# Kernel tuning notes

Hardware: AMD Instinct MI355X
Metric: run time of the kernel (lower is better)

## Reference

```python
import jax, jax.numpy as jnp
import numpy as np

N = 50000      # nodes
E = 800000     # edges (avg degree 16)
IN = 128       # in_size
OUT = 64       # out_size
H = 32         # hidden_size
WIDTH = 3      # width
SCALE = 0.05


def _laplacian(x, src, tgt, n):
    # normalized Laplacian action: out[t] = sum_{edges into t} (x[t] - x[s]) / deg(t)
    deg = jax.ops.segment_sum(jnp.ones((tgt.shape[0],), x.dtype), tgt, num_segments=n)
    fac = 1.0 / deg[tgt]                       # [E], deg>=1 for any target that appears
    msg = (x[tgt] - x[src]) * fac[:, None]     # [E, F]
    return jax.ops.segment_sum(msg, tgt, num_segments=n)


def _grouped_linear(x, Wg, bg):
    # Conv1d(kernel=1, groups=width) == per-group linear
    n = x.shape[0]
    xg = x.reshape(n, WIDTH, -1)               # [N, width, h_in]
    out = jnp.einsum('nwh,who->nwo', xg, Wg) + bg
    return out.reshape(n, -1)                  # [N, width*h_out]


def setup_inputs() -> dict:
    key = jax.random.key(0)
    ks = jax.random.split(key, 14)
    data = jax.random.normal(ks[0], (N, IN), jnp.float32)
    src = jax.random.randint(ks[1], (E,), 0, N)
    tgt = jnp.sort(jax.random.randint(ks[2], (E,), 0, N))
    # preprocess ConvSkip: Linear(in, hidden*width) + Linear(in, hidden*width)
    W_pre = jax.random.normal(ks[3], (IN, H * WIDTH), jnp.float32) * SCALE
    b_pre = jnp.zeros((H * WIDTH,), jnp.float32)
    T_pre = jax.random.normal(ks[4], (IN, H * WIDTH), jnp.float32) * SCALE
    bT_pre = jnp.zeros((H * WIDTH,), jnp.float32)
    # middle WideConvSkip (depth-2 = 1 block): grouped conv [width, H, H]
    W_blk = jax.random.normal(ks[5], (WIDTH, H, H), jnp.float32) * SCALE
    b_blk = jnp.zeros((WIDTH, H), jnp.float32)
    T_blk = jax.random.normal(ks[6], (IN, H * WIDTH), jnp.float32) * SCALE
    bT_blk = jnp.zeros((H * WIDTH,), jnp.float32)
    # postprocess WideConvSkip: grouped conv [width, H, OUT]
    W_post = jax.random.normal(ks[7], (WIDTH, H, OUT), jnp.float32) * SCALE
    b_post = jnp.zeros((WIDTH, OUT), jnp.float32)
    T_post = jax.random.normal(ks[8], (IN, OUT * WIDTH), jnp.float32) * SCALE
    bT_post = jnp.zeros((OUT * WIDTH,), jnp.float32)
    return {"data": data, "src": src, "tgt": tgt,
            "W_pre": W_pre, "b_pre": b_pre, "T_pre": T_pre, "bT_pre": bT_pre,
            "W_blk": W_blk, "b_blk": b_blk, "T_blk": T_blk, "bT_blk": bT_blk,
            "W_post": W_post, "b_post": b_post, "T_post": T_post, "bT_post": bT_post}


def reference(data, src, tgt, W_pre, b_pre, T_pre, bT_pre,
              W_blk, b_blk, T_blk, bT_blk,
              W_post, b_post, T_post, bT_post):
    n = data.shape[0]
    # preprocess ConvSkip: sigma(L f(x) + g(x))
    out = data @ W_pre + b_pre
    out = _laplacian(out, src, tgt, n)
    out = jax.nn.relu(out + data @ T_pre + bT_pre)       # [N, H*width]
    # middle WideConvSkip (depth - 2 = 1)
    h = _grouped_linear(out, W_blk, b_blk)
    h = _laplacian(h, src, tgt, n)
    out = jax.nn.relu(h + data @ T_blk + bT_blk)          # [N, H*width]
    # postprocess WideConvSkip
    h = _grouped_linear(out, W_post, b_post)
    h = _laplacian(h, src, tgt, n)
    out = jax.nn.relu(h + data @ T_post + bT_post)        # [N, OUT*width]
    # reshape(N, -1, width) then adaptive_avg_pool1d(., 1) == mean over width
    out = out.reshape(n, -1, WIDTH)
    return out.mean(axis=-1, keepdims=True)               # [N, OUT, 1]
```

## Files before the change

### kernel.cpp

```cpp
#include <hip/hip_runtime.h>
#include <hip/hip_fp8.h>
#include <cstdint>
#include <cstddef>

#define N_NODES 50000
#define E_EDGES 800000
#define IN_F    128
#define PCOLS   512

typedef unsigned short ushortT;
typedef unsigned int   uintT;
typedef unsigned char  u8T;
typedef __attribute__((ext_vector_type(8))) short s8v;
typedef __attribute__((ext_vector_type(4))) float f4v;
typedef __attribute__((ext_vector_type(2))) float f2v;

__device__ __forceinline__ float bflo(uintT u){ union{uintT i;float f;}c; c.i=u<<16; return c.f; }
__device__ __forceinline__ float bfhi(uintT u){ union{uintT i;float f;}c; c.i=u&0xFFFF0000u; return c.f; }
__device__ __forceinline__ ushortT f2bfu(float f){
    union{float f;uintT u;}c; c.f=f;
    uintT r = c.u + 0x7FFF + ((c.u>>16)&1);
    return (ushortT)(r>>16);
}
__device__ __forceinline__ uintT pack2(float a, float b){
    return (uintT)f2bfu(a) | ((uintT)f2bfu(b) << 16);
}
__device__ __forceinline__ float f8f(uintT b){
    __hip_fp8_e4m3 h; h.__x = (__hip_fp8_storage_t)(b & 0xFF); return (float)h;
}
__device__ __forceinline__ uintT ff8(float f){
    __hip_fp8_e4m3 h(f); return (uintT)h.__x;
}
__device__ __forceinline__ f2v cvtpk_sw(uintT u, bool hi){
    uintT w = hi ? (u >> 16) : u;
    f2v r; r.x = f8f(w); r.y = f8f(w >> 8); return r;
}
#if defined(__has_builtin)
#if __has_builtin(__builtin_amdgcn_cvt_pk_f32_fp8)
#define CVTPK(u, hi) __builtin_amdgcn_cvt_pk_f32_fp8((u), (hi))
#else
#define CVTPK(u, hi) cvtpk_sw((u), (hi))
#endif
#else
#define CVTPK(u, hi) cvtpk_sw((u), (hi))
#endif

__global__ void prep1(const float* __restrict__ A,
                      const float* __restrict__ Wp,  const float* __restrict__ bp,
                      const float* __restrict__ Tp,  const float* __restrict__ bTp,
                      const float* __restrict__ Tb,  const float* __restrict__ bTb,
                      const float* __restrict__ Tpo, const float* __restrict__ bTpo,
                      const float* __restrict__ Wpost,
                      const int* __restrict__ tgt,
                      ushortT* __restrict__ Wb, float* __restrict__ bcat,
                      float2* __restrict__ Wp2,
                      ushortT* __restrict__ Ab, int* __restrict__ row_ptr,
                      u8T* __restrict__ rb1f8, u8T* __restrict__ rb2f8)
{
    int gid = blockIdx.x * 256 + threadIdx.x;
    {
        size_t off = (size_t)gid * 8;
        float4 v0 = *(const float4*)(A + off);
        float4 v1 = *(const float4*)(A + off + 4);
        uint4 u;
        u.x = pack2(v0.x, v0.y); u.y = pack2(v0.z, v0.w);
        u.z = pack2(v1.x, v1.y); u.w = pack2(v1.z, v1.w);
        *(uint4*)(Ab + off) = u;
    }
    if (gid < IN_F * PCOLS) {
        int k = gid >> 9;
        int c = gid & 511;
        float v;
        if      (c < 96)  v = Wp [k*96  + c];
        else if (c < 192) v = Tp [k*96  + (c-96)];
        else if (c < 288) v = Tb [k*96  + (c-192)];
        else if (c < 480) v = Tpo[k*192 + (c-288)];
        else              v = 0.f;
        Wb[(size_t)c*IN_F + k] = f2bfu(v);
        if (k == 0) {
            float b;
            if      (c < 96)  b = bp  [c];
            else if (c < 192) b = bTp [c-96];
            else if (c < 288) b = bTb [c-192];
            else if (c < 480) b = bTpo[c-288];
            else              b = 0.f;
            bcat[c] = b;
        }
        if (gid < 3*16*64) {
            int w = gid >> 10, r = gid & 1023;
            int i2 = r >> 6, j = r & 63;
            Wp2[gid] = make_float2(Wpost[(w*32 + 2*i2)*64 + j],
                                   Wpost[(w*32 + 2*i2 + 1)*64 + j]);
        }
    }
    if (gid < 24) {
        *(uintT*)(rb1f8 + (size_t)N_NODES*96 + 4*gid) = 0;
        *(uintT*)(rb2f8 + (size_t)N_NODES*96 + 4*gid) = 0;
    }
    if (gid <= N_NODES) {
        int lo = 0, hi = E_EDGES;
        while (lo < hi) {
            int mid = (lo + hi) >> 1;
            if (tgt[mid] < gid) lo = mid + 1; else hi = mid;
        }
        row_ptr[gid] = lo;
    }
}

__global__ __launch_bounds__(256, 4) void gemm_mfma(const ushortT* __restrict__ Ab,
                                                    const ushortT* __restrict__ Wb,
                                                    const float* __restrict__ bcat,
                                                    ushortT* __restrict__ Pb, int M)
{
    __shared__ ushortT Bsl[128][136];
    int tid = threadIdx.x;
    int i = blockIdx.x;
    int xcd = i & 7, j = i >> 3;
    int nb = (j & 3) * 128;
    int mb = (xcd * 49 + (j >> 2)) * 128;
    int wv = tid >> 6, lane = tid & 63;
    int wm = wv >> 1, wn = wv & 1;
    int cl = lane & 15, q = lane >> 4;

    #pragma unroll
    for (int r = 0; r < 8; ++r) {
        int idx = tid + 256*r;
        int row = idx >> 4, qq = idx & 15;
        uint4 v = *(const uint4*)(Wb + (size_t)(nb+row)*IN_F + qq*8);
        *(uint4*)(&Bsl[row][qq*8]) = v;
    }
    __syncthreads();

    f4v acc[4][4];
    #pragma unroll
    for (int a = 0; a < 4; ++a)
        #pragma unroll
        for (int b = 0; b < 4; ++b) acc[a][b] = (f4v)0.f;

    int gmBase = mb + wm*64;
    #pragma unroll
    for (int ks = 0; ks < 4; ++ks) {
        int ko = ks*32 + q*8;
        s8v af[4], bf[4];
        #pragma unroll
        for (int mt = 0; mt < 4; ++mt) {
            int gm = gmBase + mt*16 + cl;
            uint4 va = make_uint4(0,0,0,0);
            if (gm < M) va = *(const uint4*)(Ab + (size_t)gm*IN_F + ko);
            af[mt] = *(s8v*)&va;
        }
        #pragma unroll
        for (int nt = 0; nt < 4; ++nt)
            bf[nt] = *(const s8v*)(&Bsl[wn*64 + nt*16 + cl][ko]);
        #pragma unroll
        for (int mt = 0; mt < 4; ++mt)
            #pragma unroll
            for (int nt = 0; nt < 4; ++nt)
                acc[mt][nt] = __builtin_amdgcn_mfma_f32_16x16x32_bf16(af[mt], bf[nt], acc[mt][nt], 0, 0, 0);
    }

    __syncthreads();

    #pragma unroll
    for (int nt = 0; nt < 4; ++nt) {
        int cn = wn*64 + nt*16 + cl;
        float bv = bcat[nb + cn];
        #pragma unroll
        for (int mt = 0; mt < 4; ++mt) {
            int rm0 = wm*64 + mt*16 + q*4;
            #pragma unroll
            for (int r = 0; r < 4; ++r)
                Bsl[rm0 + r][cn] = f2bfu(acc[mt][nt][r] + bv);
        }
    }
    __syncthreads();

    #pragma unroll
    for (int p = 0; p < 8; ++p) {
        int idx = tid + 256*p;
        int row = idx >> 4, sg = idx & 15;
        int gm = mb + row;
        if (gm < M) {
            uint4 v = *(const uint4*)(&Bsl[row][sg*8]);
            *(uint4*)(Pb + (size_t)gm*PCOLS + nb + sg*8) = v;
        }
    }
}

__global__ void cvt_y0(const ushortT* __restrict__ Pb, u8T* __restrict__ Y8)
{
    int gid = blockIdx.x * 256 + threadIdx.x;
    if (gid < N_NODES*24) {
        int t = gid / 24, q = gid - t*24;
        uint2 rv = *(const uint2*)(Pb + (size_t)t*PCOLS + 4*q);
        uintT o = ff8(bflo(rv.x)) | (ff8(bfhi(rv.x)) << 8)
                | (ff8(bflo(rv.y)) << 16) | (ff8(bfhi(rv.y)) << 24);
        *(uintT*)(Y8 + (size_t)t*96 + 4*q) = o;
    } else if (gid < N_NODES*24 + 24) {
        *(uintT*)(Y8 + (size_t)N_NODES*96 + 4*(gid - N_NODES*24)) = 0;
    }
}

#define LANE_GEO8                                                                 \
    int lane = threadIdx.x & 63;                                                  \
    int pL = lane < 48 ? lane : 0;                                                \
    int lq = (lane < 24) ? lane : ((lane < 48) ? lane - 24 : lane - 48);          \
    int bpb = (lane >= 24 && lane < 48) ? 4 : 0;          \
    int in4 = 4*lq;

#define GPK_W(X8, sv, S0, CNT, u)                                                 \
    _Pragma("unroll")                                                             \
    for (int s_ = 0; s_ < (CNT); ++s_) {                                          \
        int vr_ = __builtin_amdgcn_ds_bpermute(bpb + 8*((S0)+s_), sv);            \
        u[s_] = *(const uintT*)((const u8T*)(X8) + (uintT)(vr_ + in4));           \
    }
#define GPK_D(u, CNT, a0, a1, b0, b1)                                             \
    _Pragma("unroll")                                                             \
    for (int s_ = 0; s_ < (CNT); ++s_) {                                          \
        f2v l_ = CVTPK(u[s_], 0);                                                 \
        f2v h_ = CVTPK(u[s_], 1);                                                 \
        if (s_ & 1) { b0 += l_; b1 += h_; } else { a0 += l_; a1 += h_; }          \
    }
#define GATHER_PK(X8, lo, deg, sv, sx, sy)                                        \
    float sx, sy;                                                                 \
    {                                                                             \
        f2v a0={0.f,0.f}, a1={0.f,0.f}, b0={0.f,0.f}, b1={0.f,0.f};               \
        uintT u[12];                                                              \
        GPK_W(X8, sv, 0, 12, u)                                                   \
        GPK_D(u, 12, a0, a1, b0, b1)                                              \
        if (deg > 24) {                                                           \
            GPK_W(X8, sv, 12, 12, u)                                              \
            GPK_D(u, 12, a0, a1, b0, b1)                                          \
        }                                                                         \
        if (deg > 48) {                                                           \
            GPK_W(X8, sv, 24, 8, u)                                               \
            GPK_D(u, 8, a0, a1, b0, b1)                                           \
        }                                                                         \
        if (deg > 64) {                                                           \
            _Pragma("unroll 1")                                                   \
            for (int j_ = lo + 64; j_ < lo + deg; ++j_) {                         \
                int off_ = src[j_] * 96;                                          \
                uintT t_ = *(const uintT*)((const u8T*)(X8) + (uintT)(off_ + in4));\
                if (lane < 24) { a0 += CVTPK(t_, 0); a1 += CVTPK(t_, 1); }        \
            }                                                                     \
        }                                                                         \
        f2v va = a0 + b0, vb = a1 + b1;        \
         \
        int pl_ = (lane < 24) ? lane + 24 : ((lane < 48) ? lane - 24 : lane);     \
        va.x += __shfl(va.x, pl_); va.y += __shfl(va.y, pl_);                     \
        vb.x += __shfl(vb.x, pl_); vb.y += __shfl(vb.y, pl_);                     \
        int fl_ = pL >> 1;                                                        \
        float e0_ = __shfl(va.x, fl_), e1_ = __shfl(va.y, fl_);                   \
        float e2_ = __shfl(vb.x, fl_), e3_ = __shfl(vb.y, fl_);                   \
        sx = (pL & 1) ? e2_ : e0_;                                                \
        sy = (pL & 1) ? e3_ : e1_;                                                \
    }

#define DESC4(t0)                                                                 \
    int lo0,dg0,sv0, lo1,dg1,sv1, lo2,dg2,sv2, lo3,dg3,sv3;                       \
    {                                                                             \
        int rA0 = row_ptr[(t0)];    int rB0 = row_ptr[(t0)+1];                    \
        int rA1 = row_ptr[(t0)+4];  int rB1 = row_ptr[(t0)+5];                    \
        int rA2 = row_ptr[(t0)+8];  int rB2 = row_ptr[(t0)+9];                    \
        int rA3 = row_ptr[(t0)+12]; int rB3 = row_ptr[(t0)+13];                   \
        lo0 = __builtin_amdgcn_readfirstlane(rA0);                                \
        dg0 = __builtin_amdgcn_readfirstlane(rB0) - lo0;                          \
        lo1 = __builtin_amdgcn_readfirstlane(rA1);                                \
        dg1 = __builtin_amdgcn_readfirstlane(rB1) - lo1;                          \
        lo2 = __builtin_amdgcn_readfirstlane(rA2);                                \
        dg2 = __builtin_amdgcn_readfirstlane(rB2) - lo2;                          \
        lo3 = __builtin_amdgcn_readfirstlane(rA3);                                \
        dg3 = __builtin_amdgcn_readfirstlane(rB3) - lo3;                          \
        int e0 = lo0 + lane; if (e0 > E_EDGES-1) e0 = E_EDGES-1;                  \
        int e1 = lo1 + lane; if (e1 > E_EDGES-1) e1 = E_EDGES-1;                  \
        int e2 = lo2 + lane; if (e2 > E_EDGES-1) e2 = E_EDGES-1;                  \
        int e3 = lo3 + lane; if (e3 > E_EDGES-1) e3 = E_EDGES-1;                  \
        int sn0 = src[e0]; int sn1 = src[e1];                                     \
        int sn2 = src[e2]; int sn3 = src[e3];                                     \
        sv0 = (lane < dg0 ? sn0 : N_NODES) * 96;                                  \
        sv1 = (lane < dg1 ? sn1 : N_NODES) * 96;                                  \
        sv2 = (lane < dg2 ? sn2 : N_NODES) * 96;                                  \
        sv3 = (lane < dg3 ? sn3 : N_NODES) * 96;                                  \
    }

__global__ __launch_bounds__(256) void lap1(
    const ushortT* __restrict__ Pb,
    const u8T*     __restrict__ Y8,
    const int* __restrict__ src, const int* __restrict__ row_ptr,
    ushortT* __restrict__ rb1, u8T* __restrict__ rb1f8)
{
    LANE_GEO8
    int wvw = threadIdx.x >> 6;
    int t0 = blockIdx.x*16 + wvw;
    DESC4(t0)

#define LAP1_IT(tt, lo, deg, sv)                                                  \
    {                                                                             \
        int t_ = __builtin_amdgcn_readfirstlane(tt);                              \
        uintT ux = *(const uintT*)(Pb + (size_t)t_*PCOLS + 2*pL);                 \
        uintT zu = *(const uintT*)(Pb + (size_t)t_*PCOLS + 96 + 2*pL);            \
        GATHER_PK(Y8, lo, deg, sv, sx, sy)                                        \
        float inv = (deg) > 0 ? 1.f/(float)(deg) : 0.f;                           \
        float mf  = (deg) > 0 ? 1.f : 0.f;                                        \
        if (lane < 48) {                                                          \
            float ox = fmaxf(mf*bflo(ux) - sx*inv + bflo(zu), 0.f);               \
            float oy = fmaxf(mf*bfhi(ux) - sy*inv + bfhi(zu), 0.f);               \
            *(uintT*)(rb1 + (size_t)t_*96 + 2*pL) = pack2(ox, oy);                \
            *(ushortT*)(rb1f8 + (size_t)t_*96 + 2*pL) =                           \
                (ushortT)(ff8(ox) | (ff8(oy) << 8));                              \
        }                                                                         \
    }
    LAP1_IT(t0,      lo0, dg0, sv0)
    LAP1_IT(t0 + 4,  lo1, dg1, sv1)
    LAP1_IT(t0 + 8,  lo2, dg2, sv2)
    LAP1_IT(t0 + 12, lo3, dg3, sv3)
#undef LAP1_IT
}

__global__ __launch_bounds__(256) void lap2(
    const ushortT* __restrict__ Xb,
    const u8T*     __restrict__ X8,
    const ushortT* __restrict__ Pb,
    const int* __restrict__ src, const int* __restrict__ row_ptr,
    const float* __restrict__ Wblk,
    ushortT* __restrict__ rb2, u8T* __restrict__ rb2f8)
{
    __shared__ float wS[3*32*32];
    for (int i = threadIdx.x; i < 3072; i += 256) wS[i] = Wblk[i];
    __syncthreads();

    LANE_GEO8
    int wvw = threadIdx.x >> 6;
    int w  = pL >> 4;
    int jj = pL & 15;
    const float2* wc = ((const float2*)wS) + (w*512 + jj);
    int t0 = blockIdx.x*16 + wvw;
    DESC4(t0)

#define LAP2_IT(tt, lo, deg, sv)                                                  \
    {                                                                             \
        int t_ = __builtin_amdgcn_readfirstlane(tt);                              \
        uintT ux = *(const uintT*)(Xb + (size_t)t_*96 + 2*pL);                    \
        uintT zu = *(const uintT*)(Pb + (size_t)t_*PCOLS + 192 + 2*pL);           \
        GATHER_PK(X8, lo, deg, sv, sx, sy)                                        \
        float inv = (deg) > 0 ? 1.f/(float)(deg) : 0.f;                           \
        float mf  = (deg) > 0 ? 1.f : 0.f;                                        \
        float Lx = mf*bflo(ux) - sx*inv;                                          \
        float Ly = mf*bfhi(ux) - sy*inv;                                          \
        float accx = 0.f, accy = 0.f;                                             \
        _Pragma("unroll")                                                         \
        for (int d = 0; d < 16; ++d) {                                            \
            int sl = w*16 + d;                                                    \
            float ax = __shfl(Lx, sl);                                            \
            float ay = __shfl(Ly, sl);                                            \
            float2 wa = wc[(2*d)*16];                                             \
            float2 wb = wc[(2*d+1)*16];                                           \
            accx = fmaf(ax, wa.x, accx); accx = fmaf(ay, wb.x, accx);             \
            accy = fmaf(ax, wa.y, accy); accy = fmaf(ay, wb.y, accy);             \
        }                                                                         \
        if (lane < 48) {                                                          \
            float ox = fmaxf(accx + bflo(zu), 0.f);                               \
            float oy = fmaxf(accy + bfhi(zu), 0.f);                               \
            *(uintT*)(rb2 + (size_t)t_*96 + 2*pL) = pack2(ox, oy);                \
            *(ushortT*)(rb2f8 + (size_t)t_*96 + 2*pL) =                           \
                (ushortT)(ff8(ox) | (ff8(oy) << 8));                              \
        }                                                                         \
    }
    LAP2_IT(t0,      lo0, dg0, sv0)
    LAP2_IT(t0 + 4,  lo1, dg1, sv1)
    LAP2_IT(t0 + 8,  lo2, dg2, sv2)
    LAP2_IT(t0 + 12, lo3, dg3, sv3)
#undef LAP2_IT
}

__global__ __launch_bounds__(256) void lap3(
    const ushortT* __restrict__ Xb,
    const u8T*     __restrict__ X8,
    const ushortT* __restrict__ Pb,
    const int* __restrict__ src, const int* __restrict__ row_ptr,
    const float2* __restrict__ Wp2,
    float* __restrict__ out)
{
    __shared__ float2 wS[3*16*64];
    __shared__ float  sm[4][96];
    for (int i = threadIdx.x; i < 3072; i += 256) wS[i] = Wp2[i];
    __syncthreads();

    LANE_GEO8
    int wvw = threadIdx.x >> 6;
    const float2* wl = wS + lane;
    int t0 = blockIdx.x*16 + wvw;
    DESC4(t0)

#define LAP3_IT(tt, lo, deg, sv)                                                  \
    {                                                                             \
        int t_ = __builtin_amdgcn_readfirstlane(tt);                              \
        uintT ux = *(const uintT*)(Xb + (size_t)t_*96 + 2*pL);                    \
        float z0 = bflo((uintT)Pb[(size_t)t_*PCOLS + 288 + lane]);                \
        float z1 = bflo((uintT)Pb[(size_t)t_*PCOLS + 352 + lane]);                \
        float z2 = bflo((uintT)Pb[(size_t)t_*PCOLS + 416 + lane]);                \
        GATHER_PK(X8, lo, deg, sv, sx, sy)                                        \
        float inv = (deg) > 0 ? 1.f/(float)(deg) : 0.f;                           \
        float mf  = (deg) > 0 ? 1.f : 0.f;                                        \
        float Lx = mf*bflo(ux) - sx*inv;                                          \
        float Ly = mf*bfhi(ux) - sy*inv;                                          \
        if (lane < 48) {                                                          \
            sm[wvw][2*pL]     = Lx;                                               \
            sm[wvw][2*pL + 1] = Ly;                                               \
        }                                                                         \
        __builtin_amdgcn_wave_barrier();                                          \
        float a0 = 0.f, a1 = 0.f, a2 = 0.f;                                       \
        _Pragma("unroll")                                                         \
        for (int w2 = 0; w2 < 3; ++w2) {                                          \
            float acc = 0.f;                                                      \
            _Pragma("unroll")                                                     \
            for (int i2 = 0; i2 < 16; ++i2) {                                     \
                float2 iv = *(const float2*)(&sm[wvw][w2*32 + 2*i2]);             \
                float2 p  = wl[(w2*16 + i2)*64];                                  \
                acc = fmaf(iv.x, p.x, acc);                                       \
                acc = fmaf(iv.y, p.y, acc);                                       \
            }                                                                     \
            if (w2 == 0) a0 = acc; else if (w2 == 1) a1 = acc; else a2 = acc;     \
        }                                                                         \
        __builtin_amdgcn_wave_barrier();                                          \
        float o0 = fmaxf(a0 + z0, 0.f);                                           \
        float o1 = fmaxf(a1 + z1, 0.f);                                           \
        float o2 = fmaxf(a2 + z2, 0.f);                                           \
        float r = 0.f;                                                            \
        _Pragma("unroll")                                                         \
        for (int q = 0; q < 3; ++q) {                                             \
            int c = 3*lane + q;                                                   \
            int sl = c & 63, wsel = c >> 6;                                       \
            float v0 = __shfl(o0, sl);                                            \
            float v1 = __shfl(o1, sl);                                            \
            float v2 = __shfl(o2, sl);                                            \
            r += (wsel == 0) ? v0 : ((wsel == 1) ? v1 : v2);                      \
        }                                                                         \
        out[(size_t)t_*64 + lane] = r * (1.0f/3.0f);                              \
    }
    LAP3_IT(t0,      lo0, dg0, sv0)
    LAP3_IT(t0 + 4,  lo1, dg1, sv1)
    LAP3_IT(t0 + 8,  lo2, dg2, sv2)
    LAP3_IT(t0 + 12, lo3, dg3, sv3)
#undef LAP3_IT
}

extern "C" void kernel_launch(void* const* d_in, const int* in_sizes, int n_in,
                              void* d_out, int out_size, void* d_ws, size_t ws_size,
                              hipStream_t stream)
{
    const float* data    = (const float*)d_in[0];
    const int*   src     = (const int*)  d_in[1];
    const int*   tgt     = (const int*)  d_in[2];
    const float* W_pre   = (const float*)d_in[3];
    const float* b_pre   = (const float*)d_in[4];
    const float* T_pre   = (const float*)d_in[5];
    const float* bT_pre  = (const float*)d_in[6];
    const float* W_blk   = (const float*)d_in[7];
    const float* b_blk   = (const float*)d_in[8];
    const float* T_blk   = (const float*)d_in[9];
    const float* bT_blk  = (const float*)d_in[10];
    const float* W_post  = (const float*)d_in[11];
    const float* b_post  = (const float*)d_in[12];
    const float* T_post  = (const float*)d_in[13];
    const float* bT_post = (const float*)d_in[14];
    float* out = (float*)d_out;

    float*   ws      = (float*)d_ws;
    float*   bcat    = ws;
    float2*  Wp2     = (float2*)(bcat + 512);
    int*     row_ptr = (int*)(Wp2 + 3*16*64);
    ushortT* Pb      = (ushortT*)(row_ptr + 50008);
    ushortT* rb1     = Pb  + (size_t)(N_NODES+1) * PCOLS;
    ushortT* rb2     = rb1 + (size_t)(N_NODES+1) * 96;
    ushortT* Ab      = rb2 + (size_t)(N_NODES+1) * 96;
    ushortT* Wb      = Ab  + (size_t)N_NODES * IN_F;
    u8T*     Y8      = (u8T*)(Wb + 512*IN_F);
    u8T*     rb1f8   = Y8  + (size_t)(N_NODES+1) * 96;
    u8T*     rb2f8   = rb1f8 + (size_t)(N_NODES+1) * 96;

    prep1<<<(N_NODES*IN_F/8)/256, 256, 0, stream>>>(
        data, W_pre, b_pre, T_pre, bT_pre, T_blk, bT_blk, T_post, bT_post,
        W_post, tgt, Wb, bcat, Wp2, Ab, row_ptr, rb1f8, rb2f8);

    gemm_mfma<<<1568, 256, 0, stream>>>(Ab, Wb, bcat, Pb, N_NODES);

    cvt_y0<<<(N_NODES*24 + 24 + 255)/256, 256, 0, stream>>>(Pb, Y8);

    lap1<<<N_NODES/16, 256, 0, stream>>>(Pb, Y8, src, row_ptr, rb1, rb1f8);
    lap2<<<N_NODES/16, 256, 0, stream>>>(rb1, rb1f8, Pb, src, row_ptr, W_blk, rb2, rb2f8);
    lap3<<<N_NODES/16, 256, 0, stream>>>(rb2, rb2f8, Pb, src, row_ptr, Wp2, out);
}
```

Measured before the change: 269.2 us.

## Precompute padded per-node neighbor offset table and simplify fp8 gather to readlane

Adds a build_svp kernel that builds a padded [N,64] table of source-row byte offsets once, so the three Laplacian kernels load it with a coalesced read instead of recomputing src lookups each time. The gather is also rewritten: the old version split each edge across lane halves using ds_bpermute plus shuffles, and the new one has each lane load 2 bytes per edge, taking the offset via readlane and looping in chunks of 16 up to the degree. This removes the cross-lane reduction shuffles, at the cost of more, narrower loads per lane, an extra kernel launch and a 12.8 MB table that must be written and read back.

```diff
diff --git a/kernel.cpp b/kernel.cpp
--- a/kernel.cpp
+++ b/kernel.cpp
@@ -107,6 +107,18 @@
     }
 }
 
+__global__ void build_svp(const int* __restrict__ src, const int* __restrict__ row_ptr,
+                          int* __restrict__ svp)
+{
+    int gid = blockIdx.x * 256 + threadIdx.x;
+    int t = gid >> 6, slot = gid & 63;
+    int lo = row_ptr[t];
+    int deg = row_ptr[t+1] - lo;
+    int e = lo + slot; if (e > E_EDGES - 1) e = E_EDGES - 1;
+    int v = slot < deg ? src[e] : N_NODES;
+    svp[gid] = v * 96;
+}
+
 __global__ __launch_bounds__(256, 4) void gemm_mfma(const ushortT* __restrict__ Ab,
                                                     const ushortT* __restrict__ Wb,
                                                     const float* __restrict__ bcat,
@@ -201,105 +213,79 @@
     }
 }
 
-#define LANE_GEO8                                                                 \
-    int lane = threadIdx.x & 63;                                                  \
-    int pL = lane < 48 ? lane : 0;                                                \
-    int lq = (lane < 24) ? lane : ((lane < 48) ? lane - 24 : lane - 48);          \
-    int bpb = (lane >= 24 && lane < 48) ? 4 : 0;          \
-    int in4 = 4*lq;
-
-#define GPK_W(X8, sv, S0, CNT, u)                                                 \
-    _Pragma("unroll")                                                             \
-    for (int s_ = 0; s_ < (CNT); ++s_) {                                          \
-        int vr_ = __builtin_amdgcn_ds_bpermute(bpb + 8*((S0)+s_), sv);            \
-        u[s_] = *(const uintT*)((const u8T*)(X8) + (uintT)(vr_ + in4));           \
-    }
-#define GPK_D(u, CNT, a0, a1, b0, b1)                                             \
-    _Pragma("unroll")                                                             \
-    for (int s_ = 0; s_ < (CNT); ++s_) {                                          \
-        f2v l_ = CVTPK(u[s_], 0);                                                 \
-        f2v h_ = CVTPK(u[s_], 1);                                                 \
-        if (s_ & 1) { b0 += l_; b1 += h_; } else { a0 += l_; a1 += h_; }          \
-    }
-#define GATHER_PK(X8, lo, deg, sv, sx, sy)                                        \
+#define GATHER96F8(X8, lo, deg, sv, pL, sx, sy)                                   \
     float sx, sy;                                                                 \
     {                                                                             \
-        f2v a0={0.f,0.f}, a1={0.f,0.f}, b0={0.f,0.f}, b1={0.f,0.f};               \
-        uintT u[12];                                                              \
-        GPK_W(X8, sv, 0, 12, u)                                                   \
-        GPK_D(u, 12, a0, a1, b0, b1)                                              \
-        if (deg > 24) {                                                           \
-            GPK_W(X8, sv, 12, 12, u)                                              \
-            GPK_D(u, 12, a0, a1, b0, b1)                                          \
-        }                                                                         \
-        if (deg > 48) {                                                           \
-            GPK_W(X8, sv, 24, 8, u)                                               \
-            GPK_D(u, 8, a0, a1, b0, b1)                                           \
+        f2v c0={0.f,0.f}, c1={0.f,0.f}, c2={0.f,0.f}, c3={0.f,0.f};               \
+        int dmax = deg < 64 ? deg : 64;                                           \
+        _Pragma("unroll 1")                                                       \
+        for (int w_ = 0; w_ < dmax; w_ += 16) {                                   \
+            uintT u[16];                                                          \
+            _Pragma("unroll")                                                     \
+            for (int kk = 0; kk < 16; ++kk) {                                     \
+                int off = __builtin_amdgcn_readlane(sv, w_ + kk);                 \
+                u[kk] = *(const ushortT*)((const u8T*)(X8) + off + 2*pL);         \
+            }                                                                     \
+            _Pragma("unroll")                                                     \
+            for (int kk = 0; kk < 16; ++kk) {                                     \
+                f2v v_ = CVTPK(u[kk], 0);                                         \
+                switch (kk & 3) {                                                 \
+                    case 0: c0 += v_; break;                                      \
+                    case 1: c1 += v_; break;                                      \
+                    case 2: c2 += v_; break;                                      \
+                    default:c3 += v_; break;                                      \
+                }                                                                 \
+            }                                                                     \
         }                                                                         \
         if (deg > 64) {                                                           \
             _Pragma("unroll 1")                                                   \
             for (int j_ = lo + 64; j_ < lo + deg; ++j_) {                         \
-                int off_ = src[j_] * 96;                                          \
-                uintT t_ = *(const uintT*)((const u8T*)(X8) + (uintT)(off_ + in4));\
-                if (lane < 24) { a0 += CVTPK(t_, 0); a1 += CVTPK(t_, 1); }        \
+                int off = src[j_] * 96;                                           \
+                uintT u0 = *(const ushortT*)((const u8T*)(X8) + off + 2*pL);      \
+                c0 += CVTPK(u0, 0);                                               \
             }                                                                     \
         }                                                                         \
-        f2v va = a0 + b0, vb = a1 + b1;        \
-         \
-        int pl_ = (lane < 24) ? lane + 24 : ((lane < 48) ? lane - 24 : lane);     \
-        va.x += __shfl(va.x, pl_); va.y += __shfl(va.y, pl_);                     \
-        vb.x += __shfl(vb.x, pl_); vb.y += __shfl(vb.y, pl_);                     \
-        int fl_ = pL >> 1;                                                        \
-        float e0_ = __shfl(va.x, fl_), e1_ = __shfl(va.y, fl_);                   \
-        float e2_ = __shfl(vb.x, fl_), e3_ = __shfl(vb.y, fl_);                   \
-        sx = (pL & 1) ? e2_ : e0_;                                                \
-        sy = (pL & 1) ? e3_ : e1_;                                                \
-    }
-
-#define DESC4(t0)                                                                 \
-    int lo0,dg0,sv0, lo1,dg1,sv1, lo2,dg2,sv2, lo3,dg3,sv3;                       \
-    {                                                                             \
-        int rA0 = row_ptr[(t0)];    int rB0 = row_ptr[(t0)+1];                    \
-        int rA1 = row_ptr[(t0)+4];  int rB1 = row_ptr[(t0)+5];                    \
-        int rA2 = row_ptr[(t0)+8];  int rB2 = row_ptr[(t0)+9];                    \
-        int rA3 = row_ptr[(t0)+12]; int rB3 = row_ptr[(t0)+13];                   \
-        lo0 = __builtin_amdgcn_readfirstlane(rA0);                                \
-        dg0 = __builtin_amdgcn_readfirstlane(rB0) - lo0;                          \
-        lo1 = __builtin_amdgcn_readfirstlane(rA1);                                \
-        dg1 = __builtin_amdgcn_readfirstlane(rB1) - lo1;                          \
-        lo2 = __builtin_amdgcn_readfirstlane(rA2);                                \
-        dg2 = __builtin_amdgcn_readfirstlane(rB2) - lo2;                          \
-        lo3 = __builtin_amdgcn_readfirstlane(rA3);                                \
-        dg3 = __builtin_amdgcn_readfirstlane(rB3) - lo3;                          \
-        int e0 = lo0 + lane; if (e0 > E_EDGES-1) e0 = E_EDGES-1;                  \
-        int e1 = lo1 + lane; if (e1 > E_EDGES-1) e1 = E_EDGES-1;                  \
-        int e2 = lo2 + lane; if (e2 > E_EDGES-1) e2 = E_EDGES-1;                  \
-        int e3 = lo3 + lane; if (e3 > E_EDGES-1) e3 = E_EDGES-1;                  \
-        int sn0 = src[e0]; int sn1 = src[e1];                                     \
-        int sn2 = src[e2]; int sn3 = src[e3];                                     \
-        sv0 = (lane < dg0 ? sn0 : N_NODES) * 96;                                  \
-        sv1 = (lane < dg1 ? sn1 : N_NODES) * 96;                                  \
-        sv2 = (lane < dg2 ? sn2 : N_NODES) * 96;                                  \
-        sv3 = (lane < dg3 ? sn3 : N_NODES) * 96;                                  \
-    }
+        f2v cs_ = (c0 + c1) + (c2 + c3);                                          \
+        sx = cs_.x; sy = cs_.y;                                                   \
+    }
+
+#define DESC_SVP(tB)                                                              \
+    int sv0 = svp[(size_t)((tB)     )*64 + lane];                                 \
+    int sv1 = svp[(size_t)((tB) +  4)*64 + lane];                                 \
+    int sv2 = svp[(size_t)((tB) +  8)*64 + lane];                                 \
+    int sv3 = svp[(size_t)((tB) + 12)*64 + lane];                                 \
+    int rA0 = row_ptr[(tB)];    int rB0 = row_ptr[(tB)+1];                        \
+    int rA1 = row_ptr[(tB)+4];  int rB1 = row_ptr[(tB)+5];                        \
+    int rA2 = row_ptr[(tB)+8];  int rB2 = row_ptr[(tB)+9];                        \
+    int rA3 = row_ptr[(tB)+12]; int rB3 = row_ptr[(tB)+13];                       \
+    int lo0 = __builtin_amdgcn_readfirstlane(rA0);                                \
+    int dg0 = __builtin_amdgcn_readfirstlane(rB0) - lo0;                          \
+    int lo1 = __builtin_amdgcn_readfirstlane(rA1);                                \
+    int dg1 = __builtin_amdgcn_readfirstlane(rB1) - lo1;                          \
+    int lo2 = __builtin_amdgcn_readfirstlane(rA2);                                \
+    int dg2 = __builtin_amdgcn_readfirstlane(rB2) - lo2;                          \
+    int lo3 = __builtin_amdgcn_readfirstlane(rA3);                                \
+    int dg3 = __builtin_amdgcn_readfirstlane(rB3) - lo3;
 
 __global__ __launch_bounds__(256) void lap1(
     const ushortT* __restrict__ Pb,
     const u8T*     __restrict__ Y8,
     const int* __restrict__ src, const int* __restrict__ row_ptr,
+    const int* __restrict__ svp,
     ushortT* __restrict__ rb1, u8T* __restrict__ rb1f8)
 {
-    LANE_GEO8
-    int wvw = threadIdx.x >> 6;
-    int t0 = blockIdx.x*16 + wvw;
-    DESC4(t0)
+    int lane = threadIdx.x & 63;
+    int wvw  = threadIdx.x >> 6;
+    int pL = lane < 48 ? lane : 0;
+    int tB = blockIdx.x*16 + wvw;
+    DESC_SVP(tB)
 
 #define LAP1_IT(tt, lo, deg, sv)                                                  \
     {                                                                             \
         int t_ = __builtin_amdgcn_readfirstlane(tt);                              \
         uintT ux = *(const uintT*)(Pb + (size_t)t_*PCOLS + 2*pL);                 \
         uintT zu = *(const uintT*)(Pb + (size_t)t_*PCOLS + 96 + 2*pL);            \
-        GATHER_PK(Y8, lo, deg, sv, sx, sy)                                        \
+        GATHER96F8(Y8, lo, deg, sv, pL, sx, sy)                                   \
         float inv = (deg) > 0 ? 1.f/(float)(deg) : 0.f;                           \
         float mf  = (deg) > 0 ? 1.f : 0.f;                                        \
         if (lane < 48) {                                                          \
@@ -310,10 +296,10 @@
                 (ushortT)(ff8(ox) | (ff8(oy) << 8));                              \
         }                                                                         \
     }
-    LAP1_IT(t0,      lo0, dg0, sv0)
-    LAP1_IT(t0 + 4,  lo1, dg1, sv1)
-    LAP1_IT(t0 + 8,  lo2, dg2, sv2)
-    LAP1_IT(t0 + 12, lo3, dg3, sv3)
+    LAP1_IT(tB,      lo0, dg0, sv0)
+    LAP1_IT(tB + 4,  lo1, dg1, sv1)
+    LAP1_IT(tB + 8,  lo2, dg2, sv2)
+    LAP1_IT(tB + 12, lo3, dg3, sv3)
 #undef LAP1_IT
 }
 
@@ -322,27 +308,30 @@
     const u8T*     __restrict__ X8,
     const ushortT* __restrict__ Pb,
     const int* __restrict__ src, const int* __restrict__ row_ptr,
+    const int* __restrict__ svp,
     const float* __restrict__ Wblk,
     ushortT* __restrict__ rb2, u8T* __restrict__ rb2f8)
 {
     __shared__ float wS[3*32*32];
+    int lane = threadIdx.x & 63;
+    int wvw  = threadIdx.x >> 6;
+    int pL = lane < 48 ? lane : 0;
+    int tB = blockIdx.x*16 + wvw;
+    DESC_SVP(tB)
+
     for (int i = threadIdx.x; i < 3072; i += 256) wS[i] = Wblk[i];
     __syncthreads();
 
-    LANE_GEO8
-    int wvw = threadIdx.x >> 6;
     int w  = pL >> 4;
     int jj = pL & 15;
     const float2* wc = ((const float2*)wS) + (w*512 + jj);
-    int t0 = blockIdx.x*16 + wvw;
-    DESC4(t0)
 
 #define LAP2_IT(tt, lo, deg, sv)                                                  \
     {                                                                             \
         int t_ = __builtin_amdgcn_readfirstlane(tt);                              \
         uintT ux = *(const uintT*)(Xb + (size_t)t_*96 + 2*pL);                    \
         uintT zu = *(const uintT*)(Pb + (size_t)t_*PCOLS + 192 + 2*pL);           \
-        GATHER_PK(X8, lo, deg, sv, sx, sy)                                        \
+        GATHER96F8(X8, lo, deg, sv, pL, sx, sy)                                   \
         float inv = (deg) > 0 ? 1.f/(float)(deg) : 0.f;                           \
         float mf  = (deg) > 0 ? 1.f : 0.f;                                        \
         float Lx = mf*bflo(ux) - sx*inv;                                          \
@@ -366,10 +355,10 @@
                 (ushortT)(ff8(ox) | (ff8(oy) << 8));                              \
         }                                                                         \
     }
-    LAP2_IT(t0,      lo0, dg0, sv0)
-    LAP2_IT(t0 + 4,  lo1, dg1, sv1)
-    LAP2_IT(t0 + 8,  lo2, dg2, sv2)
-    LAP2_IT(t0 + 12, lo3, dg3, sv3)
+    LAP2_IT(tB,      lo0, dg0, sv0)
+    LAP2_IT(tB + 4,  lo1, dg1, sv1)
+    LAP2_IT(tB + 8,  lo2, dg2, sv2)
+    LAP2_IT(tB + 12, lo3, dg3, sv3)
 #undef LAP2_IT
 }
 
@@ -378,19 +367,22 @@
     const u8T*     __restrict__ X8,
     const ushortT* __restrict__ Pb,
     const int* __restrict__ src, const int* __restrict__ row_ptr,
+    const int* __restrict__ svp,
     const float2* __restrict__ Wp2,
     float* __restrict__ out)
 {
     __shared__ float2 wS[3*16*64];
     __shared__ float  sm[4][96];
+    int lane = threadIdx.x & 63;
+    int wvw  = threadIdx.x >> 6;
+    int pL = lane < 48 ? lane : 0;
+    int tB = blockIdx.x*16 + wvw;
+    DESC_SVP(tB)
+
     for (int i = threadIdx.x; i < 3072; i += 256) wS[i] = Wp2[i];
     __syncthreads();
 
-    LANE_GEO8
-    int wvw = threadIdx.x >> 6;
     const float2* wl = wS + lane;
-    int t0 = blockIdx.x*16 + wvw;
-    DESC4(t0)
 
 #define LAP3_IT(tt, lo, deg, sv)                                                  \
     {                                                                             \
@@ -399,7 +391,7 @@
         float z0 = bflo((uintT)Pb[(size_t)t_*PCOLS + 288 + lane]);                \
         float z1 = bflo((uintT)Pb[(size_t)t_*PCOLS + 352 + lane]);                \
         float z2 = bflo((uintT)Pb[(size_t)t_*PCOLS + 416 + lane]);                \
-        GATHER_PK(X8, lo, deg, sv, sx, sy)                                        \
+        GATHER96F8(X8, lo, deg, sv, pL, sx, sy)                                   \
         float inv = (deg) > 0 ? 1.f/(float)(deg) : 0.f;                           \
         float mf  = (deg) > 0 ? 1.f : 0.f;                                        \
         float Lx = mf*bflo(ux) - sx*inv;                                          \
@@ -438,10 +430,10 @@
         }                                                                         \
         out[(size_t)t_*64 + lane] = r * (1.0f/3.0f);                              \
     }
-    LAP3_IT(t0,      lo0, dg0, sv0)
-    LAP3_IT(t0 + 4,  lo1, dg1, sv1)
-    LAP3_IT(t0 + 8,  lo2, dg2, sv2)
-    LAP3_IT(t0 + 12, lo3, dg3, sv3)
+    LAP3_IT(tB,      lo0, dg0, sv0)
+    LAP3_IT(tB + 4,  lo1, dg1, sv1)
+    LAP3_IT(tB + 8,  lo2, dg2, sv2)
+    LAP3_IT(tB + 12, lo3, dg3, sv3)
 #undef LAP3_IT
 }
 
@@ -478,16 +470,20 @@
     u8T*     Y8      = (u8T*)(Wb + 512*IN_F);
     u8T*     rb1f8   = Y8  + (size_t)(N_NODES+1) * 96;
     u8T*     rb2f8   = rb1f8 + (size_t)(N_NODES+1) * 96;
+    int*     svp     = (int*)(rb2f8 + (size_t)(N_NODES+1) * 96 + 32);
+    svp = (int*)(((uintptr_t)svp + 15) & ~(uintptr_t)15);
 
     prep1<<<(N_NODES*IN_F/8)/256, 256, 0, stream>>>(
         data, W_pre, b_pre, T_pre, bT_pre, T_blk, bT_blk, T_post, bT_post,
         W_post, tgt, Wb, bcat, Wp2, Ab, row_ptr, rb1f8, rb2f8);
 
+    build_svp<<<(N_NODES*64)/256, 256, 0, stream>>>(src, row_ptr, svp);
+
     gemm_mfma<<<1568, 256, 0, stream>>>(Ab, Wb, bcat, Pb, N_NODES);
 
     cvt_y0<<<(N_NODES*24 + 24 + 255)/256, 256, 0, stream>>>(Pb, Y8);
 
-    lap1<<<N_NODES/16, 256, 0, stream>>>(Pb, Y8, src, row_ptr, rb1, rb1f8);
-    lap2<<<N_NODES/16, 256, 0, stream>>>(rb1, rb1f8, Pb, src, row_ptr, W_blk, rb2, rb2f8);
-    lap3<<<N_NODES/16, 256, 0, stream>>>(rb2, rb2f8, Pb, src, row_ptr, Wp2, out);
-}
+    lap1<<<N_NODES/16, 256, 0, stream>>>(Pb, Y8, src, row_ptr, svp, rb1, rb1f8);
+    lap2<<<N_NODES/16, 256, 0, stream>>>(rb1, rb1f8, Pb, src, row_ptr, svp, W_blk, rb2, rb2f8);
+    lap3<<<N_NODES/16, 256, 0, stream>>>(rb2, rb2f8, Pb, src, row_ptr, svp, Wp2, out);
+}
```

After: 265.2 us. Within noise of the previous version (-1.5%).
